# Performance work log

Measured on AMD Instinct MI355X. Metric: run time of the kernel, lower is better.

## Reference

```python
import jax, jax.numpy as jnp
import numpy as np

# dims (match init_kwargs / input_specs)
D = 768      # embed_dim
H = 12       # num query heads
G = 4        # num kv groups
E = 8        # num experts
K = 2        # experts per token
F = 4 * D    # ffn hidden dim
B, S, T = 2, 1024, 1024
DH = D // H  # head dim = 64
EPS = 1e-6


def setup_inputs() -> dict:
    key = jax.random.key(0)
    ks = jax.random.split(key, 16)

    def p(k, shape, scale=0.02):
        return jax.random.normal(k, shape, jnp.float32) * scale

    inp = {}
    inp['x'] = jax.random.normal(ks[0], (B, S, D), jnp.float32)
    inp['encoder_context'] = jax.random.normal(ks[1], (B, T, D), jnp.float32)
    for n in ('ln1', 'ln2', 'ln3'):
        inp[n + '_scale'] = jnp.ones((D,), jnp.float32)
        inp[n + '_bias'] = jnp.zeros((D,), jnp.float32)
    i = 2
    for pre in ('sa', 'ca'):
        inp[pre + '_wq'] = p(ks[i], (D, H * DH)); i += 1
        inp[pre + '_bq'] = jnp.zeros((H * DH,), jnp.float32)
        inp[pre + '_wk'] = p(ks[i], (D, G * DH)); i += 1
        inp[pre + '_bk'] = jnp.zeros((G * DH,), jnp.float32)
        inp[pre + '_wv'] = p(ks[i], (D, G * DH)); i += 1
        inp[pre + '_bv'] = jnp.zeros((G * DH,), jnp.float32)
        inp[pre + '_wo'] = p(ks[i], (H * DH, D)); i += 1
        inp[pre + '_bo'] = jnp.zeros((D,), jnp.float32)
    inp['gate_w'] = p(ks[i], (D, E)); i += 1
    inp['gate_b'] = jnp.zeros((E,), jnp.float32)
    inp['w1'] = p(ks[i], (E, D, F)); i += 1
    inp['b1'] = jnp.zeros((E, F), jnp.float32)
    inp['w2'] = p(ks[i], (E, F, D)); i += 1
    inp['b2'] = jnp.zeros((E, D), jnp.float32)
    return inp


def _ln(x, scale, bias):
    mu = jnp.mean(x, axis=-1, keepdims=True)
    var = jnp.mean(jnp.square(x - mu), axis=-1, keepdims=True)
    return (x - mu) * jax.lax.rsqrt(var + EPS) * scale + bias


def _gqa(q_in, kv_in, wq, bq, wk, bk, wv, bv, wo, bo, causal):
    Bq, Sq, _ = q_in.shape
    Skv = kv_in.shape[1]
    q = (q_in @ wq + bq).reshape(Bq, Sq, H, DH)
    k = (kv_in @ wk + bk).reshape(Bq, Skv, G, DH)
    v = (kv_in @ wv + bv).reshape(Bq, Skv, G, DH)
    rep = H // G
    k = jnp.repeat(k, rep, axis=2)  # [B,Skv,H,DH]
    v = jnp.repeat(v, rep, axis=2)
    scores = jnp.einsum('bqhd,bkhd->bhqk', q, k) / jnp.sqrt(jnp.asarray(DH, q.dtype))
    if causal:
        cmask = jnp.tril(jnp.ones((Sq, Skv), bool))
        scores = jnp.where(cmask[None, None], scores, jnp.finfo(scores.dtype).min)
    attn = jax.nn.softmax(scores, axis=-1)
    out = jnp.einsum('bhqk,bkhd->bqhd', attn, v).reshape(Bq, Sq, H * DH)
    return out @ wo + bo


def _moe(x, gate_w, gate_b, w1, b1, w2, b2):
    logits = x @ gate_w + gate_b                      # [B,S,E]
    probs = jax.nn.softmax(logits, axis=-1)
    top_v, top_i = jax.lax.top_k(probs, K)            # [B,S,K]
    top_v = top_v / jnp.sum(top_v, axis=-1, keepdims=True)
    combine = jnp.sum(jax.nn.one_hot(top_i, E, dtype=x.dtype) * top_v[..., None], axis=-2)  # [B,S,E]
    h = jax.nn.gelu(jnp.einsum('bsd,edf->ebsf', x, w1) + b1[:, None, None, :])
    y = jnp.einsum('ebsf,efd->ebsd', h, w2) + b2[:, None, None, :]
    return jnp.einsum('ebsd,bse->bsd', y, combine)


def reference(x, encoder_context,
              ln1_scale, ln1_bias, ln2_scale, ln2_bias, ln3_scale, ln3_bias,
              sa_wq, sa_bq, sa_wk, sa_bk, sa_wv, sa_bv, sa_wo, sa_bo,
              ca_wq, ca_bq, ca_wk, ca_bk, ca_wv, ca_bv, ca_wo, ca_bo,
              gate_w, gate_b, w1, b1, w2, b2):
    xn = _ln(x, ln1_scale, ln1_bias)
    x = x + _gqa(xn, xn, sa_wq, sa_bq, sa_wk, sa_bk, sa_wv, sa_bv, sa_wo, sa_bo, causal=True)
    xn = _ln(x, ln2_scale, ln2_bias)
    x = x + _gqa(xn, encoder_context, ca_wq, ca_bq, ca_wk, ca_bk, ca_wv, ca_bv, ca_wo, ca_bo, causal=False)
    xn = _ln(x, ln3_scale, ln3_bias)
    x = x + _moe(xn, gate_w, gate_b, w1, b1, w2, b2)
    return x
```

## Files before the change

### kernel.cpp

```cpp
#include <hip/hip_runtime.h>

#define DEV __device__ __forceinline__

typedef __attribute__((ext_vector_type(4))) float f32x4;
typedef __attribute__((ext_vector_type(8))) short short8;
typedef __attribute__((ext_vector_type(4))) unsigned int u32x4;
typedef __attribute__((ext_vector_type(4))) unsigned short us16x4;

#define D_ 768
#define S_ 1024
#define B_ 2
#define H_ 12
#define G_ 4
#define DH_ 64
#define E_ 8
#define F_ 3072
#define NTOK (B_*S_)

DEV unsigned short f2bf(float f){
  unsigned int b = __float_as_uint(f);
  b += 0x7FFFu + ((b >> 16) & 1u);
  return (unsigned short)(b >> 16);
}
DEV float bf2f(unsigned short h){ return __uint_as_float(((unsigned int)h) << 16); }
DEV unsigned int splitbf_pack(float v){
  unsigned short h = f2bf(v);
  unsigned short l = f2bf(v - bf2f(h));
  return (unsigned int)h | ((unsigned int)l << 16);
}

__global__ __launch_bounds__(256) void tcast_kernel(const float* __restrict__ W,
                                                    unsigned short* __restrict__ Wh,
                                                    unsigned short* __restrict__ Wl,
                                                    int K, int N){
  __shared__ float tile[32][33];
  long long zoff = (long long)blockIdx.z * K * N;
  const float* Wz = W + zoff;
  int n0 = blockIdx.x*32, k0 = blockIdx.y*32;
  int tx = threadIdx.x, ty = threadIdx.y;
  #pragma unroll
  for (int i=0;i<4;i++){
    int r = ty + i*8;
    tile[r][tx] = Wz[(long long)(k0+r)*N + n0 + tx];
  }
  __syncthreads();
  #pragma unroll
  for (int i=0;i<4;i++){
    int r = ty + i*8;
    float v = tile[tx][r];
    unsigned int hl = splitbf_pack(v);
    long long o = zoff + (long long)(n0+r)*K + k0 + tx;
    Wh[o] = (unsigned short)(hl & 0xFFFFu);
    if (Wl) Wl[o] = (unsigned short)(hl >> 16);
  }
}

__global__ void split_rows(const float* __restrict__ in, int ld, int width,
                           unsigned short* __restrict__ hi, unsigned short* __restrict__ lo){
  long long t = blockIdx.x;
  int c = threadIdx.x*4;
  f32x4 v = *(const f32x4*)(in + t*ld + c);
  unsigned int p0 = splitbf_pack(v.x), p1 = splitbf_pack(v.y);
  unsigned int p2 = splitbf_pack(v.z), p3 = splitbf_pack(v.w);
  us16x4 h, l;
  h.x=(unsigned short)p0; l.x=(unsigned short)(p0>>16);
  h.y=(unsigned short)p1; l.y=(unsigned short)(p1>>16);
  h.z=(unsigned short)p2; l.z=(unsigned short)(p2>>16);
  h.w=(unsigned short)p3; l.w=(unsigned short)(p3>>16);
  *(us16x4*)(hi + t*width + c) = h;
  *(us16x4*)(lo + t*width + c) = l;
}

__global__ void concat_bias(const float* __restrict__ b0, int n0,
                            const float* __restrict__ b1, int n1,
                            const float* __restrict__ b2, int n2,
                            float* __restrict__ out){
  int i = blockIdx.x*256 + threadIdx.x;
  if (i < n0) out[i] = b0[i];
  else if (i < n0+n1) out[i] = b1[i-n0];
  else if (i < n0+n1+n2) out[i] = b2[i-n0-n1];
}

__global__ __launch_bounds__(256) void ln_kernel(const float* __restrict__ x,
                                                 const float* __restrict__ sc,
                                                 const float* __restrict__ bi,
                                                 unsigned short* __restrict__ outh,
                                                 unsigned short* __restrict__ outl,
                                                 float* __restrict__ outf){
  __shared__ float red[8];
  long long row = blockIdx.x;
  const float* xr = x + row*D_;
  int tid = threadIdx.x;
  float v0 = xr[tid], v1 = xr[tid+256], v2 = xr[tid+512];
  float s = v0+v1+v2;
  float q = v0*v0 + v1*v1 + v2*v2;
  #pragma unroll
  for (int off=32; off; off>>=1){ s += __shfl_xor(s, off); q += __shfl_xor(q, off); }
  int lane = tid & 63, w = tid >> 6;
  if (lane == 0){ red[w] = s; red[4+w] = q; }
  __syncthreads();
  s = red[0]+red[1]+red[2]+red[3];
  q = red[4]+red[5]+red[6]+red[7];
  float mu  = s * (1.0f/D_);
  float var = q * (1.0f/D_) - mu*mu;
  float rstd = rsqrtf(var + 1e-6f);
  #pragma unroll
  for (int i=0;i<3;i++){
    int idx = tid + 256*i;
    float vv = (i==0) ? v0 : (i==1) ? v1 : v2;
    float o = (vv - mu)*rstd*sc[idx] + bi[idx];
    unsigned int pk = splitbf_pack(o);
    outh[row*D_ + idx] = (unsigned short)(pk & 0xFFFFu);
    if (outl) outl[row*D_ + idx] = (unsigned short)(pk >> 16);
    if (outf) outf[row*D_ + idx] = o;
  }
}

#define LDK 80
__global__ __launch_bounds__(256) void gemm3(
    const unsigned short* __restrict__ Ah, const unsigned short* __restrict__ Al, int lda,
    const unsigned short* __restrict__ Wh, const unsigned short* __restrict__ Wl, int K,
    const float* __restrict__ bias,
    const float* __restrict__ resid, int ldr,
    float* __restrict__ Cf, int ldc)
{
  __shared__ __align__(16) unsigned short AshH[128*LDK];
  __shared__ __align__(16) unsigned short AshL[128*LDK];
  __shared__ __align__(16) unsigned short BshH[64*LDK];
  __shared__ __align__(16) unsigned short BshL[64*LDK];
  const int r0 = blockIdx.y*128;
  const int n0 = blockIdx.x*64;
  const int tid = threadIdx.x;
  const int lane = tid & 63;
  const int wv = tid >> 6;
  const int wr = (wv>>1)*64, wc = (wv&1)*32;
  const int l15 = lane & 15, l4 = lane >> 4;

  f32x4 acc[4][2];
  #pragma unroll
  for (int i=0;i<4;i++)
    #pragma unroll
    for (int j=0;j<2;j++) acc[i][j] = (f32x4){0.f,0.f,0.f,0.f};

  for (int k0 = 0; k0 < K; k0 += 64){
    #pragma unroll
    for (int i=0;i<4;i++){
      int c = tid + i*256;
      int rr = c >> 3, kc = (c & 7)*8;
      long long src = (long long)(r0+rr)*lda + k0 + kc;
      *(u32x4*)&AshH[rr*LDK+kc] = *(const u32x4*)(Ah + src);
      *(u32x4*)&AshL[rr*LDK+kc] = *(const u32x4*)(Al + src);
    }
    #pragma unroll
    for (int i=0;i<2;i++){
      int c = tid + i*256;
      int rr = c >> 3, kc = (c & 7)*8;
      long long src = (long long)(n0+rr)*K + k0 + kc;
      *(u32x4*)&BshH[rr*LDK+kc] = *(const u32x4*)(Wh + src);
      *(u32x4*)&BshL[rr*LDK+kc] = *(const u32x4*)(Wl + src);
    }
    __syncthreads();
    #pragma unroll
    for (int ks=0; ks<2; ks++){
      int koff = ks*32 + l4*8;
      short8 bh[2], bl[2];
      #pragma unroll
      for (int fj=0; fj<2; fj++){
        bh[fj] = *(const short8*)&BshH[(wc + fj*16 + l15)*LDK + koff];
        bl[fj] = *(const short8*)&BshL[(wc + fj*16 + l15)*LDK + koff];
      }
      #pragma unroll
      for (int fi=0; fi<4; fi++){
        short8 ah = *(const short8*)&AshH[(wr + fi*16 + l15)*LDK + koff];
        short8 al = *(const short8*)&AshL[(wr + fi*16 + l15)*LDK + koff];
        #pragma unroll
        for (int fj=0; fj<2; fj++){
          acc[fi][fj] = __builtin_amdgcn_mfma_f32_16x16x32_bf16(ah, bh[fj], acc[fi][fj], 0,0,0);
          acc[fi][fj] = __builtin_amdgcn_mfma_f32_16x16x32_bf16(al, bh[fj], acc[fi][fj], 0,0,0);
          acc[fi][fj] = __builtin_amdgcn_mfma_f32_16x16x32_bf16(ah, bl[fj], acc[fi][fj], 0,0,0);
        }
      }
    }
    __syncthreads();
  }

  #pragma unroll
  for (int fi=0; fi<4; fi++)
  #pragma unroll
  for (int fj=0; fj<2; fj++)
  #pragma unroll
  for (int reg=0; reg<4; reg++){
    int r = r0 + wr + fi*16 + l4*4 + reg;
    int col = n0 + wc + fj*16 + l15;
    float val = acc[fi][fj][reg] + bias[col];
    if (resid) val += resid[(long long)r*ldr + col];
    Cf[(long long)r*ldc + col] = val;
  }
}

__global__ __launch_bounds__(256) void gemm_nt128(
    const unsigned short* __restrict__ A, int lda,
    const unsigned short* __restrict__ Wt, long long wstride,
    const float* __restrict__ bias, int bias_stride,
    const int* __restrict__ counts,
    const int* __restrict__ a_idx, int a_idx_stride,
    const int* __restrict__ row_base,
    float* __restrict__ Cf, unsigned short* __restrict__ Cb, int ldc,
    int K, int do_gelu)
{
  __shared__ __align__(16) unsigned short As[128*LDK];
  __shared__ __align__(16) unsigned short Bs[128*LDK];
  const int z = blockIdx.z;
  const int Mz = counts[z];
  const int r0 = blockIdx.y*128;
  if (r0 >= Mz) return;
  const int n0 = blockIdx.x*128;
  const int obase = row_base[z];
  const unsigned short* Wz = Wt + (long long)z*wstride;
  const float* bz = bias + (long long)z*bias_stride;
  const int tid = threadIdx.x;
  const int lane = tid & 63;
  const int wv = tid >> 6;
  const int wr = (wv>>1)*64, wc = (wv&1)*64;
  const int l15 = lane & 15, l4 = lane >> 4;

  long long arow[4];
  #pragma unroll
  for (int i=0;i<4;i++){
    int c = tid + i*256;
    int rr = c >> 3;
    int r = r0 + rr;
    int rcl = (r < Mz) ? r : (Mz-1);
    arow[i] = a_idx ? (long long)a_idx[(long long)z*a_idx_stride + rcl]
                    : (long long)(obase + rcl);
  }

  f32x4 acc[4][4];
  #pragma unroll
  for (int i=0;i<4;i++)
    #pragma unroll
    for (int j=0;j<4;j++) acc[i][j] = (f32x4){0.f,0.f,0.f,0.f};

  for (int k0 = 0; k0 < K; k0 += 64){
    #pragma unroll
    for (int i=0;i<4;i++){
      int c = tid + i*256;
      int rr = c >> 3, kc = (c & 7)*8;
      *(u32x4*)&As[rr*LDK+kc] = *(const u32x4*)(A + arow[i]*lda + k0 + kc);
      *(u32x4*)&Bs[rr*LDK+kc] = *(const u32x4*)(Wz + (long long)(n0+rr)*K + k0 + kc);
    }
    __syncthreads();
    #pragma unroll
    for (int ks=0; ks<2; ks++){
      int koff = ks*32 + l4*8;
      short8 a[4], b[4];
      #pragma unroll
      for (int f=0; f<4; f++){
        a[f] = *(const short8*)&As[(wr + f*16 + l15)*LDK + koff];
        b[f] = *(const short8*)&Bs[(wc + f*16 + l15)*LDK + koff];
      }
      #pragma unroll
      for (int fi=0; fi<4; fi++)
        #pragma unroll
        for (int fj=0; fj<4; fj++)
          acc[fi][fj] = __builtin_amdgcn_mfma_f32_16x16x32_bf16(a[fi], b[fj], acc[fi][fj], 0,0,0);
    }
    __syncthreads();
  }

  #pragma unroll
  for (int fi=0; fi<4; fi++)
  #pragma unroll
  for (int fj=0; fj<4; fj++)
  #pragma unroll
  for (int reg=0; reg<4; reg++){
    int r = r0 + wr + fi*16 + l4*4 + reg;
    if (r >= Mz) continue;
    int col = n0 + wc + fj*16 + l15;
    float val = acc[fi][fj][reg] + bz[col];
    if (do_gelu){
      float xx = val;
      float t = tanhf(0.7978845608028654f*(xx + 0.044715f*xx*xx*xx));
      val = 0.5f*xx*(1.0f + t);
    }
    long long orow = (long long)obase + r;
    if (Cf) Cf[orow*ldc + col] = val;
    if (Cb) Cb[orow*ldc + col] = f2bf(val);
  }
}

__global__ __launch_bounds__(256) void vt_split_kernel(const float* __restrict__ vin,
                                                       int ld, int cofs,
                                                       unsigned short* __restrict__ vth,
                                                       unsigned short* __restrict__ vtl){
  __shared__ float tile[32][33];
  int s0 = blockIdx.x*32, d0 = blockIdx.y*32;
  int bg = blockIdx.z; int b = bg >> 2, g = bg & 3;
  int tx = threadIdx.x, ty = threadIdx.y;
  #pragma unroll
  for (int i=0;i<4;i++){
    int r = ty + i*8;
    tile[r][tx] = vin[(long long)(b*1024 + s0 + r)*ld + cofs + g*64 + d0 + tx];
  }
  __syncthreads();
  #pragma unroll
  for (int i=0;i<4;i++){
    int d = d0 + ty + i*8;
    unsigned int pk = splitbf_pack(tile[tx][ty + i*8]);
    long long o = (long long)(bg*64 + d)*1024 + s0 + tx;
    vth[o] = (unsigned short)(pk & 0xFFFFu);
    vtl[o] = (unsigned short)(pk >> 16);
  }
}

#define AT_LDK 72
#define AT_LDP 76
__global__ __launch_bounds__(256, 2) void attn_mfma(
    const float* __restrict__ q, int qld,
    const unsigned short* __restrict__ kh, const unsigned short* __restrict__ kl,
    const unsigned short* __restrict__ vth, const unsigned short* __restrict__ vtl,
    unsigned short* __restrict__ ctxh, unsigned short* __restrict__ ctxl, int causal)
{
  __shared__ __align__(16) unsigned short KhS[64*AT_LDK];
  __shared__ __align__(16) unsigned short KlS[64*AT_LDK];
  __shared__ __align__(16) unsigned short VhS[64*AT_LDK];
  __shared__ __align__(16) unsigned short VlS[64*AT_LDK];
  __shared__ __align__(16) unsigned int   Pp[4][16*AT_LDP];

  const int qblk = blockIdx.x;
  const int h = blockIdx.y;
  const int b = blockIdx.z;
  const int g = h / (H_/G_);
  const int tid = threadIdx.x;
  const int lane = tid & 63;
  const int w = tid >> 6;
  const int l15 = lane & 15;
  const int l4 = lane >> 4;
  const int qb0 = qblk*64;

  short8 qh[2], ql[2];
  #pragma unroll
  for (int ks=0; ks<2; ks++){
    const float* qp = q + ((long long)(b*S_ + qb0 + w*16 + l15))*qld + h*DH_ + ks*32 + l4*8;
    f32x4 q0 = *(const f32x4*)qp;
    f32x4 q1 = *(const f32x4*)(qp + 4);
    float qq[8] = {q0.x,q0.y,q0.z,q0.w,q1.x,q1.y,q1.z,q1.w};
    #pragma unroll
    for (int j=0;j<8;j++){
      unsigned int pk = splitbf_pack(qq[j]*0.125f);
      qh[ks][j] = (short)(pk & 0xFFFFu);
      ql[ks][j] = (short)(pk >> 16);
    }
  }

  f32x4 o[4];
  #pragma unroll
  for (int fd=0; fd<4; fd++) o[fd] = (f32x4){0.f,0.f,0.f,0.f};
  float m[4]    = {-3.0e38f,-3.0e38f,-3.0e38f,-3.0e38f};
  float lsum[4] = {0.f,0.f,0.f,0.f};

  const int ntiles = causal ? (qblk + 1) : (S_/64);
  for (int kt=0; kt<ntiles; kt++){
    __syncthreads();
    {
      int r = tid >> 2, c = tid & 3;
      long long krow = (long long)(b*S_ + kt*64 + r)*(G_*DH_) + g*DH_;
      long long vrow = (long long)((b*G_ + g)*64 + r)*S_ + kt*64;
      *(u32x4*)&KhS[r*AT_LDK + c*8]     = *(const u32x4*)(kh + krow + c*8);
      *(u32x4*)&KhS[r*AT_LDK + (c+4)*8] = *(const u32x4*)(kh + krow + (c+4)*8);
      *(u32x4*)&KlS[r*AT_LDK + c*8]     = *(const u32x4*)(kl + krow + c*8);
      *(u32x4*)&KlS[r*AT_LDK + (c+4)*8] = *(const u32x4*)(kl + krow + (c+4)*8);
      *(u32x4*)&VhS[r*AT_LDK + c*8]     = *(const u32x4*)(vth + vrow + c*8);
      *(u32x4*)&VhS[r*AT_LDK + (c+4)*8] = *(const u32x4*)(vth + vrow + (c+4)*8);
      *(u32x4*)&VlS[r*AT_LDK + c*8]     = *(const u32x4*)(vtl + vrow + c*8);
      *(u32x4*)&VlS[r*AT_LDK + (c+4)*8] = *(const u32x4*)(vtl + vrow + (c+4)*8);
    }
    __syncthreads();

    f32x4 s[4];
    #pragma unroll
    for (int fj=0; fj<4; fj++) s[fj] = (f32x4){0.f,0.f,0.f,0.f};
    #pragma unroll
    for (int ks=0; ks<2; ks++){
      #pragma unroll
      for (int fj=0; fj<4; fj++){
        short8 bh = *(const short8*)&KhS[(fj*16 + l15)*AT_LDK + ks*32 + l4*8];
        short8 bl = *(const short8*)&KlS[(fj*16 + l15)*AT_LDK + ks*32 + l4*8];
        s[fj] = __builtin_amdgcn_mfma_f32_16x16x32_bf16(qh[ks], bh, s[fj], 0,0,0);
        s[fj] = __builtin_amdgcn_mfma_f32_16x16x32_bf16(ql[ks], bh, s[fj], 0,0,0);
        s[fj] = __builtin_amdgcn_mfma_f32_16x16x32_bf16(qh[ks], bl, s[fj], 0,0,0);
      }
    }

    if (causal && kt == qblk){
      #pragma unroll
      for (int fj=0; fj<4; fj++){
        int key = kt*64 + fj*16 + l15;
        #pragma unroll
        for (int reg=0; reg<4; reg++){
          int qr = qb0 + w*16 + l4*4 + reg;
          if (key > qr) s[fj][reg] = -3.0e38f;
        }
      }
    }

    float c[4], pmax[4];
    #pragma unroll
    for (int reg=0; reg<4; reg++){
      float mx = fmaxf(fmaxf(s[0][reg], s[1][reg]), fmaxf(s[2][reg], s[3][reg]));
      mx = fmaxf(mx, __shfl_xor(mx, 1));
      mx = fmaxf(mx, __shfl_xor(mx, 2));
      mx = fmaxf(mx, __shfl_xor(mx, 4));
      mx = fmaxf(mx, __shfl_xor(mx, 8));
      float mn = fmaxf(m[reg], mx);
      c[reg] = __expf(m[reg] - mn);
      m[reg] = mn;
      pmax[reg] = mn;
    }
    float psum[4] = {0.f,0.f,0.f,0.f};
    #pragma unroll
    for (int fj=0; fj<4; fj++){
      #pragma unroll
      for (int reg=0; reg<4; reg++){
        float pv = __expf(s[fj][reg] - pmax[reg]);
        psum[reg] += pv;
        Pp[w][(l4*4 + reg)*AT_LDP + fj*16 + l15] = splitbf_pack(pv);
      }
    }
    #pragma unroll
    for (int reg=0; reg<4; reg++){
      float ps = psum[reg];
      ps += __shfl_xor(ps, 1); ps += __shfl_xor(ps, 2);
      ps += __shfl_xor(ps, 4); ps += __shfl_xor(ps, 8);
      lsum[reg] = lsum[reg]*c[reg] + ps;
      o[0][reg] *= c[reg]; o[1][reg] *= c[reg];
      o[2][reg] *= c[reg]; o[3][reg] *= c[reg];
    }

    #pragma unroll
    for (int ks=0; ks<2; ks++){
      u32x4 pa = *(const u32x4*)&Pp[w][l15*AT_LDP + ks*32 + l4*8];
      u32x4 pb = *(const u32x4*)&Pp[w][l15*AT_LDP + ks*32 + l4*8 + 4];
      short8 ph, pl;
      #pragma unroll
      for (int j=0;j<4;j++){
        ph[j]   = (short)(pa[j] & 0xFFFFu); pl[j]   = (short)(pa[j] >> 16);
        ph[4+j] = (short)(pb[j] & 0xFFFFu); pl[4+j] = (short)(pb[j] >> 16);
      }
      #pragma unroll
      for (int fd=0; fd<4; fd++){
        short8 vh = *(const short8*)&VhS[(fd*16 + l15)*AT_LDK + ks*32 + l4*8];
        short8 vl = *(const short8*)&VlS[(fd*16 + l15)*AT_LDK + ks*32 + l4*8];
        o[fd] = __builtin_amdgcn_mfma_f32_16x16x32_bf16(ph, vh, o[fd], 0,0,0);
        o[fd] = __builtin_amdgcn_mfma_f32_16x16x32_bf16(pl, vh, o[fd], 0,0,0);
        o[fd] = __builtin_amdgcn_mfma_f32_16x16x32_bf16(ph, vl, o[fd], 0,0,0);
      }
    }
  }

  #pragma unroll
  for (int reg=0; reg<4; reg++){
    float inv = 1.0f / lsum[reg];
    long long tok = b*S_ + qb0 + w*16 + l4*4 + reg;
    #pragma unroll
    for (int fd=0; fd<4; fd++){
      unsigned int pk = splitbf_pack(o[fd][reg]*inv);
      long long oidx = tok*D_ + h*DH_ + fd*16 + l15;
      ctxh[oidx] = (unsigned short)(pk & 0xFFFFu);
      ctxl[oidx] = (unsigned short)(pk >> 16);
    }
  }
}

__global__ __launch_bounds__(256) void gate_kernel(const float* __restrict__ xnf,
                                                   const float* __restrict__ gw,
                                                   const float* __restrict__ gb,
                                                   int* __restrict__ counts,
                                                   int* __restrict__ toklist,
                                                   int* __restrict__ route_e,
                                                   int* __restrict__ route_pos,
                                                   float* __restrict__ route_w){
  int t = blockIdx.x*4 + (threadIdx.x >> 6);
  int lane = threadIdx.x & 63;
  float acc[E_];
  #pragma unroll
  for (int e=0;e<E_;e++) acc[e] = 0.f;
  #pragma unroll
  for (int i=0;i<12;i++){
    int d = lane + 64*i;
    float xv = xnf[(long long)t*D_ + d];
    const float* w = gw + (long long)d*E_;
    #pragma unroll
    for (int e=0;e<E_;e++) acc[e] += xv*w[e];
  }
  #pragma unroll
  for (int off=32; off; off>>=1)
    #pragma unroll
    for (int e=0;e<E_;e++) acc[e] += __shfl_xor(acc[e], off);
  if (lane == 0){
    #pragma unroll
    for (int e=0;e<E_;e++) acc[e] += gb[e];
    int e0 = 0;
    #pragma unroll
    for (int e=1;e<E_;e++) if (acc[e] > acc[e0]) e0 = e;
    int e1 = -1;
    #pragma unroll
    for (int e=0;e<E_;e++) if (e != e0 && (e1 < 0 || acc[e] > acc[e1])) e1 = e;
    float w0 = 1.0f/(1.0f + __expf(acc[e1] - acc[e0]));
    float w1 = 1.0f - w0;
    int p0 = atomicAdd(&counts[e0], 1);
    int p1 = atomicAdd(&counts[e1], 1);
    toklist[e0*NTOK + p0] = t;
    toklist[e1*NTOK + p1] = t;
    route_e[2*t]   = e0; route_e[2*t+1]   = e1;
    route_pos[2*t] = p0; route_pos[2*t+1] = p1;
    route_w[2*t]   = w0; route_w[2*t+1]   = w1;
  }
}

__global__ void offsets_kernel(const int* __restrict__ counts, int* __restrict__ offs){
  if (threadIdx.x == 0){
    int s = 0;
    for (int e=0;e<E_;e++){ offs[e] = s; s += counts[e]; }
  }
}

__global__ __launch_bounds__(192) void combine_kernel(const float* __restrict__ xb,
                                                      const float* __restrict__ y,
                                                      const int* __restrict__ route_e,
                                                      const int* __restrict__ route_pos,
                                                      const float* __restrict__ route_w,
                                                      const int* __restrict__ offs,
                                                      float* __restrict__ out){
  int t = blockIdx.x;
  int i = threadIdx.x;
  int e0 = route_e[2*t], e1 = route_e[2*t+1];
  long long s0 = offs[e0] + route_pos[2*t];
  long long s1 = offs[e1] + route_pos[2*t+1];
  float w0 = route_w[2*t], w1 = route_w[2*t+1];
  f32x4 xv = *(const f32x4*)(xb + (long long)t*D_ + i*4);
  f32x4 y0 = *(const f32x4*)(y + s0*D_ + i*4);
  f32x4 y1 = *(const f32x4*)(y + s1*D_ + i*4);
  f32x4 o = xv + w0*y0 + w1*y1;
  *(f32x4*)(out + (long long)t*D_ + i*4) = o;
}

extern "C" void kernel_launch(void* const* d_in, const int* in_sizes, int n_in,
                              void* d_out, int out_size, void* d_ws, size_t ws_size,
                              hipStream_t stream) {
  (void)in_sizes; (void)n_in; (void)out_size; (void)ws_size;
  const float* x     = (const float*)d_in[0];
  const float* enc   = (const float*)d_in[1];
  const float* ln1s  = (const float*)d_in[2];
  const float* ln1b  = (const float*)d_in[3];
  const float* ln2s  = (const float*)d_in[4];
  const float* ln2b  = (const float*)d_in[5];
  const float* ln3s  = (const float*)d_in[6];
  const float* ln3b  = (const float*)d_in[7];
  const float* sa_wq = (const float*)d_in[8];
  const float* sa_bq = (const float*)d_in[9];
  const float* sa_wk = (const float*)d_in[10];
  const float* sa_bk = (const float*)d_in[11];
  const float* sa_wv = (const float*)d_in[12];
  const float* sa_bv = (const float*)d_in[13];
  const float* sa_wo = (const float*)d_in[14];
  const float* sa_bo = (const float*)d_in[15];
  const float* ca_wq = (const float*)d_in[16];
  const float* ca_bq = (const float*)d_in[17];
  const float* ca_wk = (const float*)d_in[18];
  const float* ca_bk = (const float*)d_in[19];
  const float* ca_wv = (const float*)d_in[20];
  const float* ca_bv = (const float*)d_in[21];
  const float* ca_wo = (const float*)d_in[22];
  const float* ca_bo = (const float*)d_in[23];
  const float* gate_w= (const float*)d_in[24];
  const float* gate_b= (const float*)d_in[25];
  const float* w1    = (const float*)d_in[26];
  const float* b1    = (const float*)d_in[27];
  const float* w2    = (const float*)d_in[28];
  const float* b2    = (const float*)d_in[29];
  float* out = (float*)d_out;

  char* p = (char*)d_ws;
  auto alloc = [&](size_t bytes)->void*{
    void* r = (void*)p;
    p += (bytes + 255) & ~(size_t)255;
    return r;
  };
  unsigned short* wqkvh_sa = (unsigned short*)alloc((size_t)1280*768*2);
  unsigned short* wqkvl_sa = (unsigned short*)alloc((size_t)1280*768*2);
  unsigned short* woh_sa   = (unsigned short*)alloc((size_t)768*768*2);
  unsigned short* wol_sa   = (unsigned short*)alloc((size_t)768*768*2);
  unsigned short* wqh_ca   = (unsigned short*)alloc((size_t)768*768*2);
  unsigned short* wql_ca   = (unsigned short*)alloc((size_t)768*768*2);
  unsigned short* wkvh_ca  = (unsigned short*)alloc((size_t)512*768*2);
  unsigned short* wkvl_ca  = (unsigned short*)alloc((size_t)512*768*2);
  unsigned short* woh_ca   = (unsigned short*)alloc((size_t)768*768*2);
  unsigned short* wol_ca   = (unsigned short*)alloc((size_t)768*768*2);
  unsigned short* w1T = (unsigned short*)alloc((size_t)E_*D_*F_*2);
  unsigned short* w2T = (unsigned short*)alloc((size_t)E_*D_*F_*2);
  float* bqkv_sa = (float*)alloc(1280*4);
  float* bkv_ca  = (float*)alloc(512*4);
  unsigned short* ench = (unsigned short*)alloc((size_t)NTOK*D_*2);
  unsigned short* encl = (unsigned short*)alloc((size_t)NTOK*D_*2);
  unsigned short* xh   = (unsigned short*)alloc((size_t)NTOK*D_*2);
  unsigned short* xl   = (unsigned short*)alloc((size_t)NTOK*D_*2);
  unsigned short* ctxh = (unsigned short*)alloc((size_t)NTOK*D_*2);
  unsigned short* ctxl = (unsigned short*)alloc((size_t)NTOK*D_*2);
  unsigned short* xn_b = (unsigned short*)alloc((size_t)NTOK*D_*2);
  unsigned short* hbuf = (unsigned short*)alloc((size_t)2*NTOK*F_*2);
  unsigned short* khp   = (unsigned short*)alloc((size_t)NTOK*G_*DH_*2);
  unsigned short* klp   = (unsigned short*)alloc((size_t)NTOK*G_*DH_*2);
  unsigned short* vtp_h = (unsigned short*)alloc((size_t)NTOK*G_*DH_*2);
  unsigned short* vtp_l = (unsigned short*)alloc((size_t)NTOK*G_*DH_*2);
  float* qkvbuf = (float*)alloc((size_t)NTOK*1280*4);
  float* xnf  = (float*)alloc((size_t)NTOK*D_*4);
  float* xbuf = (float*)alloc((size_t)NTOK*D_*4);
  float* ybuf = (float*)alloc((size_t)2*NTOK*D_*4);
  int* counts    = (int*)alloc(E_*4);
  int* offs      = (int*)alloc(E_*4);
  int* toklist   = (int*)alloc((size_t)E_*NTOK*4);
  int* route_e   = (int*)alloc((size_t)2*NTOK*4);
  int* route_pos = (int*)alloc((size_t)2*NTOK*4);
  float* route_w = (float*)alloc((size_t)2*NTOK*4);

  (void)hipMemsetAsync(counts, 0, E_*sizeof(int), stream);

  dim3 tb(32,8);
  tcast_kernel<<<dim3(24,24,1), tb, 0, stream>>>(sa_wq, wqkvh_sa,            wqkvl_sa,            768, 768);
  tcast_kernel<<<dim3( 8,24,1), tb, 0, stream>>>(sa_wk, wqkvh_sa + 768*768,  wqkvl_sa + 768*768,  768, 256);
  tcast_kernel<<<dim3( 8,24,1), tb, 0, stream>>>(sa_wv, wqkvh_sa + 1024*768, wqkvl_sa + 1024*768, 768, 256);
  tcast_kernel<<<dim3(24,24,1), tb, 0, stream>>>(sa_wo, woh_sa, wol_sa, 768, 768);
  tcast_kernel<<<dim3(24,24,1), tb, 0, stream>>>(ca_wq, wqh_ca, wql_ca, 768, 768);
  tcast_kernel<<<dim3( 8,24,1), tb, 0, stream>>>(ca_wk, wkvh_ca,           wkvl_ca,           768, 256);
  tcast_kernel<<<dim3( 8,24,1), tb, 0, stream>>>(ca_wv, wkvh_ca + 256*768, wkvl_ca + 256*768, 768, 256);
  tcast_kernel<<<dim3(24,24,1), tb, 0, stream>>>(ca_wo, woh_ca, wol_ca, 768, 768);
  tcast_kernel<<<dim3(96,24,E_), tb, 0, stream>>>(w1, w1T, nullptr, 768, 3072);
  tcast_kernel<<<dim3(24,96,E_), tb, 0, stream>>>(w2, w2T, nullptr, 3072, 768);
  concat_bias<<<5, 256, 0, stream>>>(sa_bq, 768, sa_bk, 256, sa_bv, 256, bqkv_sa);
  concat_bias<<<2, 256, 0, stream>>>(ca_bk, 256, ca_bv, 256, nullptr, 0, bkv_ca);
  split_rows<<<NTOK, 192, 0, stream>>>(enc, 768, 768, ench, encl);

  ln_kernel<<<NTOK, 256, 0, stream>>>(x, ln1s, ln1b, xh, xl, nullptr);
  gemm3<<<dim3(20,16), 256, 0, stream>>>(xh, xl, 768, wqkvh_sa, wqkvl_sa, 768,
      bqkv_sa, nullptr, 0, qkvbuf, 1280);
  split_rows<<<NTOK, 64, 0, stream>>>(qkvbuf + 768, 1280, 256, khp, klp);
  vt_split_kernel<<<dim3(32,2,8), tb, 0, stream>>>(qkvbuf, 1280, 1024, vtp_h, vtp_l);
  attn_mfma<<<dim3(16,12,2), 256, 0, stream>>>(qkvbuf, 1280, khp, klp, vtp_h, vtp_l, ctxh, ctxl, 1);
  gemm3<<<dim3(12,16), 256, 0, stream>>>(ctxh, ctxl, 768, woh_sa, wol_sa, 768,
      sa_bo, x, 768, xbuf, 768);

  ln_kernel<<<NTOK, 256, 0, stream>>>(xbuf, ln2s, ln2b, xh, xl, nullptr);
  gemm3<<<dim3(12,16), 256, 0, stream>>>(xh, xl, 768, wqh_ca, wql_ca, 768,
      ca_bq, nullptr, 0, qkvbuf, 1280);
  gemm3<<<dim3(8,16), 256, 0, stream>>>(ench, encl, 768, wkvh_ca, wkvl_ca, 768,
      bkv_ca, nullptr, 0, qkvbuf + 768, 1280);
  split_rows<<<NTOK, 64, 0, stream>>>(qkvbuf + 768, 1280, 256, khp, klp);
  vt_split_kernel<<<dim3(32,2,8), tb, 0, stream>>>(qkvbuf, 1280, 1024, vtp_h, vtp_l);
  attn_mfma<<<dim3(16,12,2), 256, 0, stream>>>(qkvbuf, 1280, khp, klp, vtp_h, vtp_l, ctxh, ctxl, 0);
  gemm3<<<dim3(12,16), 256, 0, stream>>>(ctxh, ctxl, 768, woh_ca, wol_ca, 768,
      ca_bo, xbuf, 768, xbuf, 768);

  ln_kernel<<<NTOK, 256, 0, stream>>>(xbuf, ln3s, ln3b, xn_b, nullptr, xnf);
  gate_kernel<<<NTOK/4, 256, 0, stream>>>(xnf, gate_w, gate_b,
      counts, toklist, route_e, route_pos, route_w);
  offsets_kernel<<<1, 64, 0, stream>>>(counts, offs);
  gemm_nt128<<<dim3(24,16,E_), 256, 0, stream>>>(xn_b, 768, w1T, (long long)F_*D_, b1, F_,
      counts, toklist, NTOK, offs, nullptr, hbuf, F_, 768, 1);
  gemm_nt128<<<dim3(6,16,E_), 256, 0, stream>>>(hbuf, F_, w2T, (long long)F_*D_, b2, D_,
      counts, nullptr, 0, offs, ybuf, nullptr, 768, F_, 0);
  combine_kernel<<<NTOK, 192, 0, stream>>>(xbuf, ybuf, route_e, route_pos, route_w, offs, out);
}
```

Baseline: 539.7 us.

## Swizzle GEMM block order for XCD locality and split-K the MoE down projection

GEMM launches switch to a 1D grid decoded by an XCD-aware swizzle, so each XCD works on groups of four adjacent row blocks sharing a column panel, aiming at better L2 reuse. The second MoE GEMM is split along K into two partial outputs that the combine kernel sums, which doubles its block count to fill more CUs, at the cost of a larger y buffer and extra reads in combine. GELU's tanhf is replaced with an exp-based formula that is cheaper but slightly less accurate.

```diff
diff --git a/kernel.cpp b/kernel.cpp
--- a/kernel.cpp
+++ b/kernel.cpp
@@ -27,6 +27,15 @@
   unsigned short h = f2bf(v);
   unsigned short l = f2bf(v - bf2f(h));
   return (unsigned int)h | ((unsigned int)l << 16);
+}
+
+DEV void swz_decode(int F, int nPanels, int& m, int& panel){
+  int xcd = F & 7;
+  int a = F >> 3;
+  int mi = a & 3;
+  int pid = (a >> 2)*8 + xcd;
+  m = (pid / nPanels)*4 + mi;
+  panel = pid % nPanels;
 }
 
 __global__ __launch_bounds__(256) void tcast_kernel(const float* __restrict__ W,
@@ -118,6 +127,7 @@
 
 #define LDK 80
 __global__ __launch_bounds__(256) void gemm3(
+    int nX,
     const unsigned short* __restrict__ Ah, const unsigned short* __restrict__ Al, int lda,
     const unsigned short* __restrict__ Wh, const unsigned short* __restrict__ Wl, int K,
     const float* __restrict__ bias,
@@ -128,8 +138,10 @@
   __shared__ __align__(16) unsigned short AshL[128*LDK];
   __shared__ __align__(16) unsigned short BshH[64*LDK];
   __shared__ __align__(16) unsigned short BshL[64*LDK];
-  const int r0 = blockIdx.y*128;
-  const int n0 = blockIdx.x*64;
+  int mB, panel;
+  swz_decode(blockIdx.x, nX, mB, panel);
+  const int r0 = mB*128;
+  const int n0 = panel*64;
   const int tid = threadIdx.x;
   const int lane = tid & 63;
   const int wv = tid >> 6;
@@ -199,25 +211,33 @@
 }
 
 __global__ __launch_bounds__(256) void gemm_nt128(
+    int nX, int nzPerE,
     const unsigned short* __restrict__ A, int lda,
     const unsigned short* __restrict__ Wt, long long wstride,
     const float* __restrict__ bias, int bias_stride,
     const int* __restrict__ counts,
     const int* __restrict__ a_idx, int a_idx_stride,
     const int* __restrict__ row_base,
-    float* __restrict__ Cf, unsigned short* __restrict__ Cb, int ldc,
+    float* __restrict__ Cf, long long partStride,
+    unsigned short* __restrict__ Cb, int ldc,
     int K, int do_gelu)
 {
   __shared__ __align__(16) unsigned short As[128*LDK];
   __shared__ __align__(16) unsigned short Bs[128*LDK];
-  const int z = blockIdx.z;
+  int mB, panel;
+  swz_decode(blockIdx.x, nX*E_*nzPerE, mB, panel);
+  const int n0 = (panel % nX)*128;
+  const int zI = panel / nX;
+  const int z = zI / nzPerE;
+  const int kp = zI % nzPerE;
   const int Mz = counts[z];
-  const int r0 = blockIdx.y*128;
+  const int r0 = mB*128;
   if (r0 >= Mz) return;
-  const int n0 = blockIdx.x*128;
   const int obase = row_base[z];
   const unsigned short* Wz = Wt + (long long)z*wstride;
   const float* bz = bias + (long long)z*bias_stride;
+  const int kLen = K / nzPerE;
+  const int kBeg = kp * kLen;
   const int tid = threadIdx.x;
   const int lane = tid & 63;
   const int wv = tid >> 6;
@@ -241,7 +261,7 @@
     #pragma unroll
     for (int j=0;j<4;j++) acc[i][j] = (f32x4){0.f,0.f,0.f,0.f};
 
-  for (int k0 = 0; k0 < K; k0 += 64){
+  for (int k0 = kBeg; k0 < kBeg + kLen; k0 += 64){
     #pragma unroll
     for (int i=0;i<4;i++){
       int c = tid + i*256;
@@ -277,14 +297,15 @@
     int r = r0 + wr + fi*16 + l4*4 + reg;
     if (r >= Mz) continue;
     int col = n0 + wc + fj*16 + l15;
-    float val = acc[fi][fj][reg] + bz[col];
+    float val = acc[fi][fj][reg] + (kp == 0 ? bz[col] : 0.0f);
     if (do_gelu){
       float xx = val;
-      float t = tanhf(0.7978845608028654f*(xx + 0.044715f*xx*xx*xx));
+      float u = 0.7978845608028654f*(xx + 0.044715f*xx*xx*xx);
+      float t = 1.0f - 2.0f/(__expf(2.0f*u) + 1.0f);
       val = 0.5f*xx*(1.0f + t);
     }
     long long orow = (long long)obase + r;
-    if (Cf) Cf[orow*ldc + col] = val;
+    if (Cf) Cf[kp*partStride + orow*ldc + col] = val;
     if (Cb) Cb[orow*ldc + col] = f2bf(val);
   }
 }
@@ -527,6 +548,7 @@
 
 __global__ __launch_bounds__(192) void combine_kernel(const float* __restrict__ xb,
                                                       const float* __restrict__ y,
+                                                      long long partStride,
                                                       const int* __restrict__ route_e,
                                                       const int* __restrict__ route_pos,
                                                       const float* __restrict__ route_w,
@@ -538,10 +560,12 @@
   long long s0 = offs[e0] + route_pos[2*t];
   long long s1 = offs[e1] + route_pos[2*t+1];
   float w0 = route_w[2*t], w1 = route_w[2*t+1];
-  f32x4 xv = *(const f32x4*)(xb + (long long)t*D_ + i*4);
-  f32x4 y0 = *(const f32x4*)(y + s0*D_ + i*4);
-  f32x4 y1 = *(const f32x4*)(y + s1*D_ + i*4);
-  f32x4 o = xv + w0*y0 + w1*y1;
+  f32x4 xv  = *(const f32x4*)(xb + (long long)t*D_ + i*4);
+  f32x4 y0a = *(const f32x4*)(y + s0*D_ + i*4);
+  f32x4 y0b = *(const f32x4*)(y + partStride + s0*D_ + i*4);
+  f32x4 y1a = *(const f32x4*)(y + s1*D_ + i*4);
+  f32x4 y1b = *(const f32x4*)(y + partStride + s1*D_ + i*4);
+  f32x4 o = xv + w0*(y0a + y0b) + w1*(y1a + y1b);
   *(f32x4*)(out + (long long)t*D_ + i*4) = o;
 }
 
@@ -616,7 +640,7 @@
   float* qkvbuf = (float*)alloc((size_t)NTOK*1280*4);
   float* xnf  = (float*)alloc((size_t)NTOK*D_*4);
   float* xbuf = (float*)alloc((size_t)NTOK*D_*4);
-  float* ybuf = (float*)alloc((size_t)2*NTOK*D_*4);
+  float* ybuf = (float*)alloc((size_t)4*NTOK*D_*4);
   int* counts    = (int*)alloc(E_*4);
   int* offs      = (int*)alloc(E_*4);
   int* toklist   = (int*)alloc((size_t)E_*NTOK*4);
@@ -642,32 +666,34 @@
   split_rows<<<NTOK, 192, 0, stream>>>(enc, 768, 768, ench, encl);
 
   ln_kernel<<<NTOK, 256, 0, stream>>>(x, ln1s, ln1b, xh, xl, nullptr);
-  gemm3<<<dim3(20,16), 256, 0, stream>>>(xh, xl, 768, wqkvh_sa, wqkvl_sa, 768,
+  gemm3<<<20*16, 256, 0, stream>>>(20, xh, xl, 768, wqkvh_sa, wqkvl_sa, 768,
       bqkv_sa, nullptr, 0, qkvbuf, 1280);
   split_rows<<<NTOK, 64, 0, stream>>>(qkvbuf + 768, 1280, 256, khp, klp);
   vt_split_kernel<<<dim3(32,2,8), tb, 0, stream>>>(qkvbuf, 1280, 1024, vtp_h, vtp_l);
   attn_mfma<<<dim3(16,12,2), 256, 0, stream>>>(qkvbuf, 1280, khp, klp, vtp_h, vtp_l, ctxh, ctxl, 1);
-  gemm3<<<dim3(12,16), 256, 0, stream>>>(ctxh, ctxl, 768, woh_sa, wol_sa, 768,
+  gemm3<<<12*16, 256, 0, stream>>>(12, ctxh, ctxl, 768, woh_sa, wol_sa, 768,
       sa_bo, x, 768, xbuf, 768);
 
   ln_kernel<<<NTOK, 256, 0, stream>>>(xbuf, ln2s, ln2b, xh, xl, nullptr);
-  gemm3<<<dim3(12,16), 256, 0, stream>>>(xh, xl, 768, wqh_ca, wql_ca, 768,
+  gemm3<<<12*16, 256, 0, stream>>>(12, xh, xl, 768, wqh_ca, wql_ca, 768,
       ca_bq, nullptr, 0, qkvbuf, 1280);
-  gemm3<<<dim3(8,16), 256, 0, stream>>>(ench, encl, 768, wkvh_ca, wkvl_ca, 768,
+  gemm3<<<8*16, 256, 0, stream>>>(8, ench, encl, 768, wkvh_ca, wkvl_ca, 768,
       bkv_ca, nullptr, 0, qkvbuf + 768, 1280);
   split_rows<<<NTOK, 64, 0, stream>>>(qkvbuf + 768, 1280, 256, khp, klp);
   vt_split_kernel<<<dim3(32,2,8), tb, 0, stream>>>(qkvbuf, 1280, 1024, vtp_h, vtp_l);
   attn_mfma<<<dim3(16,12,2), 256, 0, stream>>>(qkvbuf, 1280, khp, klp, vtp_h, vtp_l, ctxh, ctxl, 0);
-  gemm3<<<dim3(12,16), 256, 0, stream>>>(ctxh, ctxl, 768, woh_ca, wol_ca, 768,
+  gemm3<<<12*16, 256, 0, stream>>>(12, ctxh, ctxl, 768, woh_ca, wol_ca, 768,
       ca_bo, xbuf, 768, xbuf, 768);
 
   ln_kernel<<<NTOK, 256, 0, stream>>>(xbuf, ln3s, ln3b, xn_b, nullptr, xnf);
   gate_kernel<<<NTOK/4, 256, 0, stream>>>(xnf, gate_w, gate_b,
       counts, toklist, route_e, route_pos, route_w);
   offsets_kernel<<<1, 64, 0, stream>>>(counts, offs);
-  gemm_nt128<<<dim3(24,16,E_), 256, 0, stream>>>(xn_b, 768, w1T, (long long)F_*D_, b1, F_,
-      counts, toklist, NTOK, offs, nullptr, hbuf, F_, 768, 1);
-  gemm_nt128<<<dim3(6,16,E_), 256, 0, stream>>>(hbuf, F_, w2T, (long long)F_*D_, b2, D_,
-      counts, nullptr, 0, offs, ybuf, nullptr, 768, F_, 0);
-  combine_kernel<<<NTOK, 192, 0, stream>>>(xbuf, ybuf, route_e, route_pos, route_w, offs, out);
-}
+  gemm_nt128<<<24*16*E_, 256, 0, stream>>>(24, 1, xn_b, 768, w1T, (long long)F_*D_, b1, F_,
+      counts, toklist, NTOK, offs, nullptr, 0, hbuf, F_, 768, 1);
+  long long partStride = (long long)2*NTOK*D_;
+  gemm_nt128<<<6*16*E_*2, 256, 0, stream>>>(6, 2, hbuf, F_, w2T, (long long)F_*D_, b2, D_,
+      counts, nullptr, 0, offs, ybuf, partStride, nullptr, 768, F_, 0);
+  combine_kernel<<<NTOK, 192, 0, stream>>>(xbuf, ybuf, partStride,
+      route_e, route_pos, route_w, offs, out);
+}
```

Result: no change. 534.4 us (-1.0%).
